# Optimization experiments

Measured on AMD Instinct MI355X. Metric: run time of the kernel, lower is better.

Reference implementation:

```python
import jax, jax.numpy as jnp
import numpy as np

S_GRID = 7
B_BOX = 2
N_CLS = 20
N_CH = B_BOX * 5 + N_CLS  # 30
LAMBDA_OBJ = 5.0
LAMBDA_NOOBJ = 0.5
CI = np.array([4, 9])
BI = np.array([0, 1, 2, 3, 5, 6, 7, 8])


def setup_inputs() -> dict:
    key = jax.random.key(0)
    k1, k2 = jax.random.split(key)
    batch = 512
    P = jax.random.uniform(k1, (batch, S_GRID, S_GRID, N_CH), dtype=jnp.float32)
    T = jax.random.uniform(k2, (batch, S_GRID, S_GRID, N_CH), dtype=jnp.float32)
    # deterministic object mask: 1/8 of cells are 'object' cells (channel 4 == 1 exactly)
    cell_idx = jnp.arange(batch * S_GRID * S_GRID).reshape(batch, S_GRID, S_GRID)
    obj_mask = (cell_idx % 8 == 0).astype(jnp.float32)
    T = T.at[..., 4].set(obj_mask)
    return {"P": P, "T": T}


def _norm2dnorm(b, S):
    # (cx, cy, w, h) -> (x1, y1, x2, y2) with cx,cy divided by S
    xy = b[:, :2] / S
    wh = b[:, 2:]
    return jnp.concatenate([xy - 0.5 * wh, xy + 0.5 * wh], axis=-1)


def _iou_mat(b1, b2):
    # b1: (N,4), b2: (M,4) -> (N,M) IoU
    lt = jnp.maximum(b1[:, None, :2], b2[None, :, :2])
    rb = jnp.minimum(b1[:, None, 2:], b2[None, :, 2:])
    wh = jnp.clip(rb - lt, 0.0)
    inter = wh[..., 0] * wh[..., 1]
    a1 = (b1[:, 2] - b1[:, 0]) * (b1[:, 3] - b1[:, 1])
    a2 = (b2[:, 2] - b2[:, 0]) * (b2[:, 3] - b2[:, 1])
    return inter / (a1[:, None] + a2[None, :] - inter)


def reference(P, T):
    batch = P.shape[0]
    Pf = P.reshape(-1, N_CH)
    Tf = T.reshape(-1, N_CH)
    # masks computed on concrete data (static counts by construction)
    obj = np.asarray(Tf[:, 4] == 1.0)
    coord_idx = jnp.asarray(np.nonzero(obj)[0])
    noobj_idx = jnp.asarray(np.nonzero(~obj)[0])

    coordP = Pf[coord_idx]
    coordT = Tf[coord_idx]
    noobjP = Pf[noobj_idx]
    noobjT = Tf[noobj_idx]

    ClassP = coordP[:, B_BOX * 5:]
    ClassT = coordT[:, B_BOX * 5:]
    NoObjP = noobjP[:, CI].reshape(-1)
    NoObjT = noobjT[:, CI].reshape(-1)
    ConfP = coordP[:, CI].reshape(-1)          # (2*Ncoord,)
    BBoxP = coordP[:, BI].reshape(-1, 4)       # (2*Ncoord, 4)
    BBoxT = coordT[:, BI].reshape(-1, 4)

    # original torch code does this under no_grad -> stop_gradient
    BP = jax.lax.stop_gradient(_norm2dnorm(BBoxP, float(S_GRID)))
    BT = jax.lax.stop_gradient(_norm2dnorm(BBoxT, float(S_GRID)))
    M = _iou_mat(BP, BT)                       # (NSize, NSize)
    iou = jax.lax.stop_gradient(jnp.max(M, axis=0))
    idx = jnp.argmax(M, axis=0)                # best pred row per target column

    BPg = BP[idx]
    BTg = BT[idx]
    ConfPg = ConfP[idx]

    lossXY = jnp.sum((BPg[:, :2] - BTg[:, :2]) ** 2)
    lossWH = jnp.sum((jnp.sqrt(BPg[:, 2:]) - jnp.sqrt(BTg[:, 2:])) ** 2)
    lossObj = jnp.sum((ConfPg - iou) ** 2)
    lossNObj = jnp.sum((NoObjP - NoObjT) ** 2)
    lossClass = jnp.sum((ClassP - ClassT) ** 2)

    return (LAMBDA_OBJ * (lossXY + lossWH) + LAMBDA_NOOBJ * lossNObj + (lossObj + lossClass)) / batch
```

## Files before the change

### kernel.cpp

```cpp
#include <hip/hip_runtime.h>
#include <stdint.h>

#define S_GRID 7
#define N_CH 30
#define MAXB 8192
#define NTILE 32
#define NCHUNK 80
#define CHUNK_MAX 104


__global__ void k_init(float* __restrict__ acc, int* __restrict__ ctr, int* __restrict__ finalCtr) {
    if (threadIdx.x < 4)  acc[threadIdx.x] = 0.0f;
    if (threadIdx.x == 4) *ctr = 0;
    if (threadIdx.x == 5) *finalCtr = 0;
}

__global__ void k_prep(const float* __restrict__ P, const float* __restrict__ T, int ncell,
                       int* __restrict__ ctr,
                       float4* __restrict__ PB4, float4* __restrict__ BT4,
                       float* __restrict__ ConfP,
                       float* __restrict__ acc,
                       unsigned long long* __restrict__ maxkey) {
    int gid = blockIdx.x * 256 + threadIdx.x;
    if (gid < MAXB) maxkey[gid] = 0ull;

    int cell = gid;
    float2 pr[15], tr[15];
    if (cell < ncell) {
        const float2* p2 = (const float2*)(P + (size_t)cell * N_CH);
        const float2* t2 = (const float2*)(T + (size_t)cell * N_CH);
        #pragma unroll
        for (int k = 0; k < 15; ++k) { pr[k] = p2[k]; tr[k] = t2[k]; }
    } else {
        #pragma unroll
        for (int k = 0; k < 15; ++k) { pr[k] = make_float2(0.f, 0.f); tr[k] = make_float2(0.f, 0.f); }
    }
    bool obj = (cell < ncell) && (tr[2].x == 1.0f);

    int lane = threadIdx.x & 63;
    unsigned long long bm = __ballot(obj);
    int wcnt = __popcll(bm);
    int base = 0;
    if (lane == 0 && wcnt) base = atomicAdd(ctr, wcnt);
    base = __shfl(base, 0);

    float cls = 0.f, nob = 0.f;
    if (cell < ncell) {
        if (obj) {
            #pragma unroll
            for (int k = 5; k < 15; ++k) {
                float d0 = pr[k].x - tr[k].x, d1 = pr[k].y - tr[k].y;
                cls += d0 * d0 + d1 * d1;
            }
        } else {
            float d0 = pr[2].x - tr[2].x;
            float d1 = pr[4].y - tr[4].y;
            nob = d0 * d0 + d1 * d1;
        }
    }
    #pragma unroll
    for (int o = 32; o; o >>= 1) { cls += __shfl_down(cls, o); nob += __shfl_down(nob, o); }
    if (lane == 0) {
        if (cls != 0.f) atomicAdd(&acc[3], cls);
        if (nob != 0.f) atomicAdd(&acc[2], nob);
    }

    if (obj) {
        int rank = base + __popcll(bm & ((1ull << lane) - 1ull));
        float bx[2][5] = {
            { pr[0].x, pr[0].y, pr[1].x, pr[1].y, pr[2].x },
            { pr[2].y, pr[3].x, pr[3].y, pr[4].x, pr[4].y }
        };
        float tx[2][4] = {
            { tr[0].x, tr[0].y, tr[1].x, tr[1].y },
            { tr[2].y, tr[3].x, tr[3].y, tr[4].x }
        };
        #pragma unroll
        for (int bb = 0; bb < 2; ++bb) {
            int m = 2 * rank + bb;
            if (m < MAXB) {
                float cx = bx[bb][0] / (float)S_GRID, cy = bx[bb][1] / (float)S_GRID;
                float w = bx[bb][2], h = bx[bb][3];
                PB4[m] = make_float4(cx - 0.5f * w, cy - 0.5f * h, cx + 0.5f * w, cy + 0.5f * h);
                ConfP[m] = bx[bb][4];
                cx = tx[bb][0] / (float)S_GRID; cy = tx[bb][1] / (float)S_GRID;
                w = tx[bb][2]; h = tx[bb][3];
                BT4[m] = make_float4(cx - 0.5f * w, cy - 0.5f * h, cx + 0.5f * w, cy + 0.5f * h);
            }
        }
    }
}

__global__ void k_match(const float4* __restrict__ PB4, const float4* __restrict__ BT4,
                        const int* __restrict__ ctr,
                        unsigned long long* __restrict__ maxkey) {
    __shared__ float4 sh[CHUNK_MAX];
    int nb = 2 * (*ctr); if (nb > MAXB) nb = MAXB;
    int tid = threadIdx.x;
    int j = blockIdx.x * 256 + tid;
    if (blockIdx.x * 256 >= nb) return;
    int c = blockIdx.y;
    int chunkLen = (((nb + NCHUNK - 1) / NCHUNK) + 3) & ~3;
    int i0 = c * chunkLen;
    int i1 = min(nb, i0 + chunkLen);
    if (i0 >= i1) return;

    int len = i1 - i0;
    int padded = (len + 3) & ~3;
    for (int k = tid; k < padded; k += 256)
        sh[k] = (k < len) ? PB4[i0 + k] : make_float4(0.f, 0.f, 0.f, 0.f);
    __syncthreads();

    float4 tb = BT4[min(j, nb - 1)];
    float ta = (tb.z - tb.x) * (tb.w - tb.y);
    float bI = -1.f, bS = 1.f;
    int bidx = 0;

    for (int kb = 0; kb < padded; kb += 4) {
        float4 b0 = sh[kb], b1 = sh[kb + 1], b2 = sh[kb + 2], b3 = sh[kb + 3];
        #define STEP(bb, kk)  {                                                     \
            float lx = fmaxf(tb.x, bb.x), ly = fmaxf(tb.y, bb.y);                   \
            float rx = fminf(tb.z, bb.z), ry = fminf(tb.w, bb.w);                   \
            float wx = fmaxf(rx - lx, 0.f), wy = fmaxf(ry - ly, 0.f);               \
            float inter = wx * wy;                                                  \
            float area = (bb.z - bb.x) * (bb.w - bb.y);                             \
            float sum = ta + area;                                                  \
            bool win = (inter * bS > bI * sum) && ((kb + kk) < len);                \
            bI   = win ? inter          : bI;                                       \
            bS   = win ? sum            : bS;                                       \
            bidx = win ? (i0 + kb + kk) : bidx;                                     \
        }
        STEP(b0, 0) STEP(b1, 1) STEP(b2, 2) STEP(b3, 3)
        #undef STEP
    }

    if (j < nb && bI >= 0.f) {
        float iou = bI / (bS - bI);
        unsigned long long key =
            ((unsigned long long)__float_as_uint(iou) << 32) |
            (unsigned long long)(0xFFFFFFFFu - (unsigned)bidx);
        atomicMax(&maxkey[j], key);
    }
}

__global__ void k_final(const float4* __restrict__ PB4, const float4* __restrict__ BT4,
                        const float* __restrict__ ConfP,
                        const int* __restrict__ ctr,
                        const unsigned long long* __restrict__ maxkey,
                        float* __restrict__ acc, int* __restrict__ finalCtr,
                        float* __restrict__ out, float inv_batch) {
    int nb = 2 * (*ctr); if (nb > MAXB) nb = MAXB;
    int tid = threadIdx.x;
    int j = blockIdx.x * 256 + tid;
    float sxywh = 0.f, sobj = 0.f;
    if (j < nb) {
        unsigned long long key = maxkey[j];
        float iou = __uint_as_float((unsigned)(key >> 32));
        unsigned idx = 0xFFFFFFFFu - (unsigned)(key & 0xFFFFFFFFull);
        float4 bp = PB4[idx];
        float4 bt = BT4[idx];
        float cp = ConfP[idx];
        float dx = bp.x - bt.x, dy = bp.y - bt.y;
        float dw = sqrtf(bp.z) - sqrtf(bt.z);
        float dh = sqrtf(bp.w) - sqrtf(bt.w);
        sxywh = dx * dx + dy * dy + dw * dw + dh * dh;
        float dob = cp - iou;
        sobj = dob * dob;
    }
    #pragma unroll
    for (int o = 32; o; o >>= 1) { sxywh += __shfl_down(sxywh, o); sobj += __shfl_down(sobj, o); }
    if ((tid & 63) == 0) {
        if (sxywh != 0.f) atomicAdd(&acc[0], sxywh);
        if (sobj != 0.f)  atomicAdd(&acc[1], sobj);
    }
    __syncthreads();
    if (tid == 0) {
        int old = __hip_atomic_fetch_add(finalCtr, 1, __ATOMIC_ACQ_REL, __HIP_MEMORY_SCOPE_AGENT);
        if (old == NTILE - 1) {
            float a0 = __hip_atomic_load(&acc[0], __ATOMIC_RELAXED, __HIP_MEMORY_SCOPE_AGENT);
            float a1 = __hip_atomic_load(&acc[1], __ATOMIC_RELAXED, __HIP_MEMORY_SCOPE_AGENT);
            float a2 = __hip_atomic_load(&acc[2], __ATOMIC_RELAXED, __HIP_MEMORY_SCOPE_AGENT);
            float a3 = __hip_atomic_load(&acc[3], __ATOMIC_RELAXED, __HIP_MEMORY_SCOPE_AGENT);
            out[0] = (5.0f * a0 + 0.5f * a2 + a1 + a3) * inv_batch;
        }
    }
}

extern "C" void kernel_launch(void* const* d_in, const int* in_sizes, int n_in,
                              void* d_out, int out_size, void* d_ws, size_t ws_size,
                              hipStream_t stream) {
    const float* P = (const float*)d_in[0];
    const float* T = (const float*)d_in[1];
    int ncell = in_sizes[0] / N_CH;
    int batch = ncell / (S_GRID * S_GRID);

    char* ws = (char*)d_ws;
    float* acc      = (float*)ws;
    int*   ctr      = (int*)(ws + 16);
    int*   finalCtr = (int*)(ws + 20);
    unsigned long long* maxkey = (unsigned long long*)(ws + 1024);
    float4* PB4  = (float4*)(ws + 66560);
    float4* BT4  = (float4*)(ws + 197632);
    float*  ConfP = (float*)(ws + 328704);

    int nblk = (ncell + 255) / 256;
    k_init <<<1, 64, 0, stream>>>(acc, ctr, finalCtr);
    k_prep <<<nblk, 256, 0, stream>>>(P, T, ncell, ctr, PB4, BT4, ConfP, acc, maxkey);
    dim3 g3(NTILE, NCHUNK);
    k_match<<<g3, 256, 0, stream>>>(PB4, BT4, ctr, maxkey);
    k_final<<<NTILE, 256, 0, stream>>>(PB4, BT4, ConfP, ctr, maxkey, acc, finalCtr,
                                       (float*)d_out, 1.0f / (float)batch);
}
```

Before: 57.49 us.

## Replace global atomics with per-chunk partial keys and fold init into prep

```diff
diff --git a/kernel.cpp b/kernel.cpp
--- a/kernel.cpp
+++ b/kernel.cpp
@@ -5,24 +5,23 @@
 #define N_CH 30
 #define MAXB 8192
 #define NTILE 32
-#define NCHUNK 80
-#define CHUNK_MAX 104
-
-
-__global__ void k_init(float* __restrict__ acc, int* __restrict__ ctr, int* __restrict__ finalCtr) {
-    if (threadIdx.x < 4)  acc[threadIdx.x] = 0.0f;
-    if (threadIdx.x == 4) *ctr = 0;
-    if (threadIdx.x == 5) *finalCtr = 0;
-}
+#define NCHUNK 32
+#define CHUNK_MAX 256
+
 
 __global__ void k_prep(const float* __restrict__ P, const float* __restrict__ T, int ncell,
                        int* __restrict__ ctr,
                        float4* __restrict__ PB4, float4* __restrict__ BT4,
                        float* __restrict__ ConfP,
-                       float* __restrict__ acc,
-                       unsigned long long* __restrict__ maxkey) {
-    int gid = blockIdx.x * 256 + threadIdx.x;
-    if (gid < MAXB) maxkey[gid] = 0ull;
+                       float* __restrict__ pcls, float* __restrict__ pnobj,
+                       float* __restrict__ acc, int* __restrict__ finalCtr) {
+    int b = blockIdx.x, tid = threadIdx.x;
+    int gid = b * 256 + tid;
+
+    if (b == 0) {
+        if (tid < 4)  acc[tid] = 0.0f;
+        if (tid == 4) *finalCtr = 0;
+    }
 
     int cell = gid;
     float2 pr[15], tr[15];
@@ -37,7 +36,7 @@
     }
     bool obj = (cell < ncell) && (tr[2].x == 1.0f);
 
-    int lane = threadIdx.x & 63;
+    int lane = tid & 63, wid = tid >> 6;
     unsigned long long bm = __ballot(obj);
     int wcnt = __popcll(bm);
     int base = 0;
@@ -60,9 +59,12 @@
     }
     #pragma unroll
     for (int o = 32; o; o >>= 1) { cls += __shfl_down(cls, o); nob += __shfl_down(nob, o); }
-    if (lane == 0) {
-        if (cls != 0.f) atomicAdd(&acc[3], cls);
-        if (nob != 0.f) atomicAdd(&acc[2], nob);
+    __shared__ float shC[4], shN[4];
+    if (lane == 0) { shC[wid] = cls; shN[wid] = nob; }
+    __syncthreads();
+    if (tid == 0) {
+        pcls[b]  = shC[0] + shC[1] + shC[2] + shC[3];
+        pnobj[b] = shN[0] + shN[1] + shN[2] + shN[3];
     }
 
     if (obj) {
@@ -93,7 +95,7 @@
 
 __global__ void k_match(const float4* __restrict__ PB4, const float4* __restrict__ BT4,
                         const int* __restrict__ ctr,
-                        unsigned long long* __restrict__ maxkey) {
+                        unsigned long long* __restrict__ pkeys) {
     __shared__ float4 sh[CHUNK_MAX];
     int nb = 2 * (*ctr); if (nb > MAXB) nb = MAXB;
     int tid = threadIdx.x;
@@ -108,16 +110,19 @@
     int len = i1 - i0;
     int padded = (len + 3) & ~3;
     for (int k = tid; k < padded; k += 256)
-        sh[k] = (k < len) ? PB4[i0 + k] : make_float4(0.f, 0.f, 0.f, 0.f);
+        sh[k] = (k < len) ? PB4[i0 + k] : make_float4(3.f, 3.f, 3.f, 3.f);
     __syncthreads();
 
     float4 tb = BT4[min(j, nb - 1)];
     float ta = (tb.z - tb.x) * (tb.w - tb.y);
     float bI = -1.f, bS = 1.f;
-    int bidx = 0;
-
+    int bidx = i0;
+
+    float4 n0 = sh[0], n1 = sh[1], n2 = sh[2], n3 = sh[3];
     for (int kb = 0; kb < padded; kb += 4) {
-        float4 b0 = sh[kb], b1 = sh[kb + 1], b2 = sh[kb + 2], b3 = sh[kb + 3];
+        float4 b0 = n0, b1 = n1, b2 = n2, b3 = n3;
+        int nx = kb + 4;
+        if (nx < padded) { n0 = sh[nx]; n1 = sh[nx + 1]; n2 = sh[nx + 2]; n3 = sh[nx + 3]; }
         #define STEP(bb, kk)  {                                                     \
             float lx = fmaxf(tb.x, bb.x), ly = fmaxf(tb.y, bb.y);                   \
             float rx = fminf(tb.z, bb.z), ry = fminf(tb.w, bb.w);                   \
@@ -125,7 +130,7 @@
             float inter = wx * wy;                                                  \
             float area = (bb.z - bb.x) * (bb.w - bb.y);                             \
             float sum = ta + area;                                                  \
-            bool win = (inter * bS > bI * sum) && ((kb + kk) < len);                \
+            bool win = (inter * bS > bI * sum);                                     \
             bI   = win ? inter          : bI;                                       \
             bS   = win ? sum            : bS;                                       \
             bidx = win ? (i0 + kb + kk) : bidx;                                     \
@@ -134,19 +139,20 @@
         #undef STEP
     }
 
-    if (j < nb && bI >= 0.f) {
-        float iou = bI / (bS - bI);
+    if (j < nb) {
+        float iou = (bI >= 0.f) ? (bI / (bS - bI)) : 0.f;
         unsigned long long key =
             ((unsigned long long)__float_as_uint(iou) << 32) |
             (unsigned long long)(0xFFFFFFFFu - (unsigned)bidx);
-        atomicMax(&maxkey[j], key);
+        pkeys[(size_t)c * MAXB + j] = key;
     }
 }
 
 __global__ void k_final(const float4* __restrict__ PB4, const float4* __restrict__ BT4,
                         const float* __restrict__ ConfP,
                         const int* __restrict__ ctr,
-                        const unsigned long long* __restrict__ maxkey,
+                        const unsigned long long* __restrict__ pkeys,
+                        const float* __restrict__ pcls, const float* __restrict__ pnobj, int nblk,
                         float* __restrict__ acc, int* __restrict__ finalCtr,
                         float* __restrict__ out, float inv_batch) {
     int nb = 2 * (*ctr); if (nb > MAXB) nb = MAXB;
@@ -154,7 +160,14 @@
     int j = blockIdx.x * 256 + tid;
     float sxywh = 0.f, sobj = 0.f;
     if (j < nb) {
-        unsigned long long key = maxkey[j];
+        int chunkLen = (((nb + NCHUNK - 1) / NCHUNK) + 3) & ~3;
+        unsigned long long key = 0;
+        #pragma unroll 4
+        for (int c = 0; c < NCHUNK; ++c) {
+            if (c * chunkLen >= nb) break;
+            unsigned long long k2 = pkeys[(size_t)c * MAXB + j];
+            if (k2 > key) key = k2;
+        }
         float iou = __uint_as_float((unsigned)(key >> 32));
         unsigned idx = 0xFFFFFFFFu - (unsigned)(key & 0xFFFFFFFFull);
         float4 bp = PB4[idx];
@@ -167,11 +180,19 @@
         float dob = cp - iou;
         sobj = dob * dob;
     }
+    float exC = 0.f, exN = 0.f;
+    if (blockIdx.x == 0 && tid < nblk) { exC = pcls[tid]; exN = pnobj[tid]; }
+
     #pragma unroll
-    for (int o = 32; o; o >>= 1) { sxywh += __shfl_down(sxywh, o); sobj += __shfl_down(sobj, o); }
+    for (int o = 32; o; o >>= 1) {
+        sxywh += __shfl_down(sxywh, o); sobj += __shfl_down(sobj, o);
+        exC   += __shfl_down(exC, o);   exN  += __shfl_down(exN, o);
+    }
     if ((tid & 63) == 0) {
         if (sxywh != 0.f) atomicAdd(&acc[0], sxywh);
         if (sobj != 0.f)  atomicAdd(&acc[1], sobj);
+        if (exN != 0.f)   atomicAdd(&acc[2], exN);
+        if (exC != 0.f)   atomicAdd(&acc[3], exC);
     }
     __syncthreads();
     if (tid == 0) {
@@ -196,18 +217,22 @@
 
     char* ws = (char*)d_ws;
     float* acc      = (float*)ws;
-    int*   ctr      = (int*)(ws + 16);
-    int*   finalCtr = (int*)(ws + 20);
-    unsigned long long* maxkey = (unsigned long long*)(ws + 1024);
-    float4* PB4  = (float4*)(ws + 66560);
-    float4* BT4  = (float4*)(ws + 197632);
-    float*  ConfP = (float*)(ws + 328704);
+    int*   finalCtr = (int*)(ws + 16);
+    float* pcls     = (float*)(ws + 64);
+    float* pnobj    = (float*)(ws + 576);
+    int*   ctr      = (int*)(ws + 1024);
+    float4* PB4  = (float4*)(ws + 4096);
+    float4* BT4  = (float4*)(ws + 135168);
+    float*  ConfP = (float*)(ws + 266240);
+    unsigned long long* pkeys = (unsigned long long*)(ws + 299008);
+
+    hipMemsetAsync(ctr, 0, 4, stream);
 
     int nblk = (ncell + 255) / 256;
-    k_init <<<1, 64, 0, stream>>>(acc, ctr, finalCtr);
-    k_prep <<<nblk, 256, 0, stream>>>(P, T, ncell, ctr, PB4, BT4, ConfP, acc, maxkey);
+    k_prep <<<nblk, 256, 0, stream>>>(P, T, ncell, ctr, PB4, BT4, ConfP,
+                                      pcls, pnobj, acc, finalCtr);
     dim3 g3(NTILE, NCHUNK);
-    k_match<<<g3, 256, 0, stream>>>(PB4, BT4, ctr, maxkey);
-    k_final<<<NTILE, 256, 0, stream>>>(PB4, BT4, ConfP, ctr, maxkey, acc, finalCtr,
-                                       (float*)d_out, 1.0f / (float)batch);
-}
+    k_match<<<g3, 256, 0, stream>>>(PB4, BT4, ctr, pkeys);
+    k_final<<<NTILE, 256, 0, stream>>>(PB4, BT4, ConfP, ctr, pkeys, pcls, pnobj, nblk,
+                                       acc, finalCtr, (float*)d_out, 1.0f / (float)batch);
+}
```

Result: slower. 59.02 us (+2.6%).
